# Kernel optimization log

Hardware: AMD Instinct MI355X
Metric: run time of the kernel (lower is better)

Reference implementation:

```python
import jax, jax.numpy as jnp
import numpy as np

B, S, E, NUM_CLASSES = 4, 4096, 256, 16

def setup_inputs() -> dict:
    key = jax.random.key(0)
    ks = jax.random.split(key, 10)
    std = E ** -0.5
    return {
        "x":  jax.random.normal(ks[0], (B, S, E), dtype=jnp.float32),
        "wq": jax.random.normal(ks[1], (E, E), dtype=jnp.float32) * std,
        "bq": jnp.zeros((E,), dtype=jnp.float32),
        "wk": jax.random.normal(ks[2], (E, E), dtype=jnp.float32) * std,
        "bk": jnp.zeros((E,), dtype=jnp.float32),
        "wv": jax.random.normal(ks[3], (E, E), dtype=jnp.float32) * std,
        "bv": jnp.zeros((E,), dtype=jnp.float32),
        "wo": jax.random.normal(ks[4], (NUM_CLASSES, E), dtype=jnp.float32) * std,
        "bo": jnp.zeros((NUM_CLASSES,), dtype=jnp.float32),
    }

def reference(x, wq, bq, wk, bk, wv, bv, wo, bo):
    embed_dim = wq.shape[0]
    scaling = embed_dim ** -0.5  # float(embed_dim) ** (-0.5)
    # torch Linear: y = x @ W.T + b
    Q = jnp.einsum('bse,oe->bso', x, wq) + bq
    K = jnp.einsum('bse,oe->bso', x, wk) + bk
    V = jnp.einsum('bse,oe->bso', x, wv) + bv
    # scores: [B, S, S]
    scores = jnp.einsum('bqe,bke->bqk', Q, K) * scaling
    # original code has `/ (embed_dim ^ 0.5)`; intended math is / sqrt(embed_dim)
    attn = jax.nn.softmax(scores, axis=-1) * scaling
    attn_out = jnp.einsum('bqk,bke->bqe', attn, V)
    return jnp.einsum('bqe,oe->bqo', attn_out, wo) + bo
```

## Files before the change

### kernel.cpp

```cpp
#include <hip/hip_runtime.h>
#include <hip/hip_bf16.h>


#define S_ 4096
#define E_ 256
#define B_ 4
#define NC_ 16
#define BS_ (B_ * S_)
#define NS_ 4

typedef __attribute__((ext_vector_type(8))) short bf16x8;
typedef __attribute__((ext_vector_type(4))) float f32x4;

__device__ __forceinline__ unsigned short bf16_rtne(float f) {
    unsigned int u = __float_as_uint(f);
    return (unsigned short)((u + 0x7FFFu + ((u >> 16) & 1u)) >> 16);
}
__device__ __forceinline__ bf16x8 pack8(f32x4 a, f32x4 b) {
    bf16x8 r;
#pragma unroll
    for (int i = 0; i < 4; i++) r[i] = (short)bf16_rtne(a[i]);
#pragma unroll
    for (int i = 0; i < 4; i++) r[4 + i] = (short)bf16_rtne(b[i]);
    return r;
}
__device__ __forceinline__ void gl_lds16(const void* g, void* lds) {
    __builtin_amdgcn_global_load_lds(
        (const __attribute__((address_space(1))) unsigned int*)g,
        (__attribute__((address_space(3))) unsigned int*)lds, 16, 0, 0);
}
__device__ __forceinline__ int swz_u(int q) { return q ^ ((q >> 3) & 7); }

#define WUNITS_ (3 * E_ * E_ / 8)
#define WOUNITS_ (NC_ * E_ / 8)
#define ZUNITS_ (BS_ * NC_ / 8)
__global__ __launch_bounds__(256) void pack_w(
    const float* __restrict__ wq, const float* __restrict__ wk,
    const float* __restrict__ wv, const float* __restrict__ wo,
    short* __restrict__ wb, short* __restrict__ wbo,
    float* __restrict__ partial) {
    int u = blockIdx.x * 256 + threadIdx.x;
    const float* src;
    short* dst;
    if (u < WUNITS_) {
        int sel = u >> 13;
        int off = (u & 8191) * 8;
        src = ((sel == 0) ? wq : (sel == 1) ? wk : wv) + off;
        dst = wb + sel * (E_ * E_) + off;
    } else if (u < WUNITS_ + WOUNITS_) {
        int u2 = u - WUNITS_;
        src = wo + (size_t)u2 * 8;
        dst = wbo + (size_t)u2 * 8;
    } else {
        int zu = u - (WUNITS_ + WOUNITS_);
        f32x4 z = {0.f, 0.f, 0.f, 0.f};
        ((f32x4*)partial)[zu * 2] = z;
        ((f32x4*)partial)[zu * 2 + 1] = z;
        return;
    }
    f32x4 a = *(const f32x4*)src;
    f32x4 b = *(const f32x4*)(src + 4);
    *(bf16x8*)dst = pack8(a, b);
}

__global__ __launch_bounds__(256) void qkv_gemm(
    const float* __restrict__ x, const short* __restrict__ wb,
    const float* __restrict__ bq, const float* __restrict__ bk,
    const float* __restrict__ bv, short* __restrict__ Qb,
    short* __restrict__ Kb, short* __restrict__ Vtc) {
    __shared__ __align__(16) short stg[2][8192];
    __shared__ __align__(16) short epi[16896];

    int t = threadIdx.x;
    int lin = blockIdx.x;
    int xcd = lin & 7, r8 = lin >> 3;
    int sel = r8 >> 5;
    int m0 = (((xcd << 5) | (r8 & 31))) * 64;
    int lane = t & 63, wid = t >> 6, quad = lane >> 4, idx = lane & 15;

    const short* wsel = wb + sel * (E_ * E_);
    const float* bias = (sel == 0) ? bq : (sel == 1) ? bk : bv;

    const short* wsrc[4];
#pragma unroll
    for (int i = 0; i < 4; i++) {
        int q = i * 256 + t, u = swz_u(q);
        wsrc[i] = wsel + (size_t)(u >> 2) * E_ + (u & 3) * 8;
    }

#pragma unroll
    for (int i = 0; i < 4; i++) gl_lds16(wsrc[i], &stg[0][(i * 256 + t) * 8]);

    const float* xrow = x + (size_t)(m0 + wid * 16 + idx) * E_ + quad * 8;
    bf16x8 af[8];
#pragma unroll
    for (int it = 0; it < 8; it++) {
        f32x4 a0 = *(const f32x4*)(xrow + it * 32);
        f32x4 a1 = *(const f32x4*)(xrow + it * 32 + 4);
        af[it] = pack8(a0, a1);
    }

    f32x4 zf = {0.f, 0.f, 0.f, 0.f};
    f32x4 acc[16];
#pragma unroll
    for (int i = 0; i < 16; i++) acc[i] = zf;

    int fo = (idx * 4 + quad) ^ (idx >> 1);

#pragma unroll
    for (int it = 0; it < 8; it++) {
        __syncthreads();
        if (it < 7) {
            int kc = (it + 1) * 32;
            short* d = stg[(it + 1) & 1];
#pragma unroll
            for (int i = 0; i < 4; i++)
                gl_lds16(wsrc[i] + kc, &d[(i * 256 + t) * 8]);
        }
        const short* cw = &stg[it & 1][fo * 8];
        __builtin_amdgcn_s_setprio(1);
#pragma unroll
        for (int ct = 0; ct < 16; ct++)
            acc[ct] = __builtin_amdgcn_mfma_f32_16x16x32_bf16(
                af[it], *(const bf16x8*)&cw[ct * 512], acc[ct], 0, 0, 0);
        __builtin_amdgcn_s_setprio(0);
    }

    int qr = quad * 4;
    if (sel == 2) {
#pragma unroll
        for (int ct = 0; ct < 16; ct++) {
            int e = ct * 16 + idx;
            float bb = bias[e];
#pragma unroll
            for (int r = 0; r < 4; r++) {
                int mr = wid * 16 + qr + r;
                int ckg = mr >> 5, sin = mr & 31;
                int sp = ((sin & 15) << 1) | (sin >> 4);
                int pos = (sp >> 3) ^ ((e >> 1) & 3);
                epi[ckg * 8192 + e * 32 + pos * 8 + (sp & 7)] =
                    (short)bf16_rtne(acc[ct][r] + bb);
            }
        }
        __syncthreads();
        size_t base = ((size_t)((m0 >> 12) * 128 + ((m0 & (S_ - 1)) >> 5))) * 8192;
#pragma unroll
        for (int j = 0; j < 8; j++) {
            int unit = j * 256 + t;
            *(bf16x8*)(Vtc + base + (size_t)unit * 8) = *(const bf16x8*)&epi[unit * 8];
        }
    } else {
        float alpha = (sel == 0) ? 0.0625f : 1.0f;
#pragma unroll
        for (int ct = 0; ct < 16; ct++) {
            int n = ct * 16 + idx;
            float bb = bias[n];
#pragma unroll
            for (int r = 0; r < 4; r++) {
                int row = wid * 16 + qr + r;
                int col = (sel == 1) ? ((((n >> 3) ^ (row & 7)) << 3) | (n & 7)) : n;
                epi[row * 264 + col] = (short)bf16_rtne((acc[ct][r] + bb) * alpha);
            }
        }
        __syncthreads();
        short* out = (sel == 0) ? Qb : Kb;
#pragma unroll
        for (int j = 0; j < 8; j++) {
            int g = j * 256 + t;
            int row = g >> 5, seg = g & 31;
            *(bf16x8*)(out + (size_t)(m0 + row) * E_ + seg * 8) =
                *(const bf16x8*)&epi[row * 264 + seg * 8];
        }
    }
}

__global__ __launch_bounds__(256, 2) void flash_attn(
    const short* __restrict__ Qb, const short* __restrict__ Kb,
    const short* __restrict__ Vtc, const short* __restrict__ wbo,
    float* __restrict__ partial, float* __restrict__ lpart) {
    __shared__ __align__(16) short lds[37888];

    int t = threadIdx.x;
    int lin = blockIdx.x;
    int xcd = lin & 7, r8 = lin >> 3;
    int pair = (xcd << 1) | (r8 >> 5);
    int b = pair >> 2, slice = pair & 3, q0 = (r8 & 31) * 128;
    int key0 = slice * (S_ / NS_);
    const int nchunk = (S_ / NS_) / 32;
    int lane = t & 63, wv = t >> 6, quad = lane >> 4, idx = lane & 15;

    bf16x8 qf[2][8];
#pragma unroll
    for (int u = 0; u < 2; u++) {
        const short* qrow = Qb + (size_t)(b * S_ + q0 + u * 64 + wv * 16 + idx) * E_ + quad * 8;
#pragma unroll
        for (int c = 0; c < 8; c++) qf[u][c] = *(const bf16x8*)(qrow + c * 32);
    }

    f32x4 zf = {0.f, 0.f, 0.f, 0.f};
    f32x4 oacc[2][16];
#pragma unroll
    for (int u = 0; u < 2; u++)
#pragma unroll
        for (int i = 0; i < 16; i++) oacc[u][i] = zf;
    float ls[2][4] = {{0, 0, 0, 0}, {0, 0, 0, 0}};

    const short* kg = Kb + (size_t)(b * S_ + key0) * E_ + lane * 8;
    const short* vg = Vtc + ((size_t)(b * 128 + (key0 >> 5))) * 8192 + lane * 8;
    short* psw = lds + 32768 + wv * 1280;
    unsigned int* pswu = (unsigned int*)psw;
    int vsw = (quad ^ ((idx >> 1) & 3)) << 3;

#pragma unroll
    for (int j = 0; j < 4; j++) gl_lds16(kg + (wv * 4 + j) * 512, &lds[(wv * 4 + j) * 512]);
#pragma unroll
    for (int j = 0; j < 4; j++) gl_lds16(vg + (wv * 4 + j) * 512, &lds[16384 + (wv * 4 + j) * 512]);
#pragma unroll
    for (int j = 0; j < 4; j++) gl_lds16(kg + 8192 + (wv * 4 + j) * 512, &lds[8192 + (wv * 4 + j) * 512]);
    __syncthreads();

    {
        f32x4 s[4] = {zf, zf, zf, zf};
        __builtin_amdgcn_s_setprio(1);
#pragma unroll
        for (int c = 0; c < 8; c++) {
            int p = (((c * 4 + quad) ^ (idx & 7)) << 3);
            bf16x8 k0 = *(const bf16x8*)&lds[idx * 256 + p];
            bf16x8 k1 = *(const bf16x8*)&lds[(16 + idx) * 256 + p];
            s[0] = __builtin_amdgcn_mfma_f32_16x16x32_bf16(qf[0][c], k0, s[0], 0, 0, 0);
            s[1] = __builtin_amdgcn_mfma_f32_16x16x32_bf16(qf[0][c], k1, s[1], 0, 0, 0);
            s[2] = __builtin_amdgcn_mfma_f32_16x16x32_bf16(qf[1][c], k0, s[2], 0, 0, 0);
            s[3] = __builtin_amdgcn_mfma_f32_16x16x32_bf16(qf[1][c], k1, s[3], 0, 0, 0);
        }
        __builtin_amdgcn_s_setprio(0);
#pragma unroll
        for (int u = 0; u < 2; u++)
#pragma unroll
            for (int r = 0; r < 4; r++) {
                float p0 = __expf(s[u * 2][r]);
                float p1 = __expf(s[u * 2 + 1][r]);
                ls[u][r] += p0 + p1;
                pswu[u * 320 + (quad * 4 + r) * 20 + idx] =
                    (unsigned int)bf16_rtne(p0) | ((unsigned int)bf16_rtne(p1) << 16);
            }
    }

    for (int ck = 0; ck < nchunk - 1; ck++) {
        __syncthreads();
        bf16x8 af0 = *(const bf16x8*)&psw[idx * 40 + quad * 8];
        bf16x8 af1 = *(const bf16x8*)&psw[640 + idx * 40 + quad * 8];
        if (ck + 2 < nchunk) {
            const short* ks = kg + (size_t)(ck + 2) * 8192;
            short* kd = lds + (ck & 1) * 8192;
#pragma unroll
            for (int j = 0; j < 4; j++) gl_lds16(ks + (wv * 4 + j) * 512, &kd[(wv * 4 + j) * 512]);
        }
        {
            const short* vs = vg + (size_t)(ck + 1) * 8192;
            short* vd = lds + 16384 + ((ck + 1) & 1) * 8192;
#pragma unroll
            for (int j = 0; j < 4; j++) gl_lds16(vs + (wv * 4 + j) * 512, &vd[(wv * 4 + j) * 512]);
        }
        const short* kc = lds + ((ck + 1) & 1) * 8192;
        f32x4 s[4] = {zf, zf, zf, zf};
        __builtin_amdgcn_s_setprio(1);
#pragma unroll
        for (int c = 0; c < 8; c++) {
            int p = (((c * 4 + quad) ^ (idx & 7)) << 3);
            bf16x8 k0 = *(const bf16x8*)&kc[idx * 256 + p];
            bf16x8 k1 = *(const bf16x8*)&kc[(16 + idx) * 256 + p];
            s[0] = __builtin_amdgcn_mfma_f32_16x16x32_bf16(qf[0][c], k0, s[0], 0, 0, 0);
            s[1] = __builtin_amdgcn_mfma_f32_16x16x32_bf16(qf[0][c], k1, s[1], 0, 0, 0);
            s[2] = __builtin_amdgcn_mfma_f32_16x16x32_bf16(qf[1][c], k0, s[2], 0, 0, 0);
            s[3] = __builtin_amdgcn_mfma_f32_16x16x32_bf16(qf[1][c], k1, s[3], 0, 0, 0);
        }
        __builtin_amdgcn_s_setprio(0);
#pragma unroll
        for (int u = 0; u < 2; u++)
#pragma unroll
            for (int r = 0; r < 4; r++) {
                float p0 = __expf(s[u * 2][r]);
                float p1 = __expf(s[u * 2 + 1][r]);
                ls[u][r] += p0 + p1;
                pswu[u * 320 + (quad * 4 + r) * 20 + idx] =
                    (unsigned int)bf16_rtne(p0) | ((unsigned int)bf16_rtne(p1) << 16);
            }
        const short* vc = lds + 16384 + (ck & 1) * 8192;
        __builtin_amdgcn_s_setprio(1);
#pragma unroll
        for (int ct = 0; ct < 16; ct++) {
            bf16x8 v = *(const bf16x8*)&vc[(ct * 16 + idx) * 32 + vsw];
            oacc[0][ct] = __builtin_amdgcn_mfma_f32_16x16x32_bf16(af0, v, oacc[0][ct], 0, 0, 0);
            oacc[1][ct] = __builtin_amdgcn_mfma_f32_16x16x32_bf16(af1, v, oacc[1][ct], 0, 0, 0);
        }
        __builtin_amdgcn_s_setprio(0);
    }
    __syncthreads();
    {
        bf16x8 af0 = *(const bf16x8*)&psw[idx * 40 + quad * 8];
        bf16x8 af1 = *(const bf16x8*)&psw[640 + idx * 40 + quad * 8];
        const short* vc = lds + 16384 + ((nchunk - 1) & 1) * 8192;
        __builtin_amdgcn_s_setprio(1);
#pragma unroll
        for (int ct = 0; ct < 16; ct++) {
            bf16x8 v = *(const bf16x8*)&vc[(ct * 16 + idx) * 32 + vsw];
            oacc[0][ct] = __builtin_amdgcn_mfma_f32_16x16x32_bf16(af0, v, oacc[0][ct], 0, 0, 0);
            oacc[1][ct] = __builtin_amdgcn_mfma_f32_16x16x32_bf16(af1, v, oacc[1][ct], 0, 0, 0);
        }
        __builtin_amdgcn_s_setprio(0);
    }
    __syncthreads();

#pragma unroll
    for (int u = 0; u < 2; u++)
#pragma unroll
        for (int r = 0; r < 4; r++) {
            float v = ls[u][r];
            v += __shfl_xor(v, 1);
            v += __shfl_xor(v, 2);
            v += __shfl_xor(v, 4);
            v += __shfl_xor(v, 8);
            if (idx == 0)
                lpart[(size_t)slice * BS_ + b * S_ + q0 + u * 64 + wv * 16 + quad * 4 + r] = v;
        }

    short* scr = lds + wv * 8192;
#pragma unroll
    for (int u = 0; u < 2; u++)
#pragma unroll
        for (int ct = 0; ct < 16; ct++) {
            int e = ct * 16 + idx;
#pragma unroll
            for (int r = 0; r < 4; r++) {
                int lr = quad * 4 + r;
                scr[u * 4096 + lr * 256 + ((((e >> 3) ^ (lr & 7)) << 3) | (e & 7))] =
                    (short)bf16_rtne(oacc[u][ct][r]);
            }
        }

    f32x4 pacc[2] = {zf, zf};
#pragma unroll
    for (int c = 0; c < 8; c++) {
        bf16x8 bw = *(const bf16x8*)(wbo + idx * E_ + c * 32 + quad * 8);
#pragma unroll
        for (int u = 0; u < 2; u++) {
            bf16x8 af = *(const bf16x8*)&scr[u * 4096 + idx * 256 +
                                             (((c * 4 + quad) ^ (idx & 7)) << 3)];
            pacc[u] = __builtin_amdgcn_mfma_f32_16x16x32_bf16(af, bw, pacc[u], 0, 0, 0);
        }
    }
#pragma unroll
    for (int u = 0; u < 2; u++)
#pragma unroll
        for (int r = 0; r < 4; r++) {
            int m = q0 + u * 64 + wv * 16 + quad * 4 + r;
            atomicAdd(&partial[((size_t)b * S_ + m) * NC_ + idx], pacc[u][r]);
        }
}

__global__ __launch_bounds__(256) void norm_out(
    const float* __restrict__ partial, const float* __restrict__ lpart,
    const float* __restrict__ bo, float* __restrict__ out) {
    int t = threadIdx.x;
    int m = blockIdx.x * 16 + (t >> 4), o = t & 15;
    float ltot = 0.f;
#pragma unroll
    for (int ns = 0; ns < NS_; ns++) ltot += lpart[(size_t)ns * BS_ + m];
    size_t i = (size_t)m * NC_ + o;
    out[i] = partial[i] * (0.0625f / ltot) + bo[o];
}

extern "C" void kernel_launch(void* const* d_in, const int* in_sizes, int n_in,
                              void* d_out, int out_size, void* d_ws, size_t ws_size,
                              hipStream_t stream) {
    const float* x  = (const float*)d_in[0];
    const float* wq = (const float*)d_in[1];
    const float* bq = (const float*)d_in[2];
    const float* wk = (const float*)d_in[3];
    const float* bk = (const float*)d_in[4];
    const float* wv = (const float*)d_in[5];
    const float* bv = (const float*)d_in[6];
    const float* wo = (const float*)d_in[7];
    const float* bo = (const float*)d_in[8];
    float* out = (float*)d_out;

    const size_t NEL = (size_t)BS_ * E_;
    short* Qb = (short*)d_ws;
    short* Kb = Qb + NEL;
    short* Vtc = Kb + NEL;
    short* wb = Vtc + NEL;
    short* wbo = wb + (size_t)3 * E_ * E_;
    float* partial = (float*)(wbo + (size_t)NC_ * E_);
    float* lpart = partial + (size_t)BS_ * NC_;

    pack_w<<<(WUNITS_ + WOUNITS_ + ZUNITS_) / 256, 256, 0, stream>>>(
        wq, wk, wv, wo, wb, wbo, partial);
    qkv_gemm<<<dim3(768), 256, 0, stream>>>(x, wb, bq, bk, bv, Qb, Kb, Vtc);
    flash_attn<<<dim3(512), 256, 0, stream>>>(Qb, Kb, Vtc, wbo, partial, lpart);
    norm_out<<<dim3(BS_ / 16), 256, 0, stream>>>(partial, lpart, bo, out);
}
```

Measured before the change: 169.9 us.

## Double query tile per flash-attention block to 256 rows for more K/V reuse

Each flash_attn block now handles 256 query rows (4 sub-tiles per wave) instead of 128, which halves the grid to 256 blocks and sets launch bounds to 1 block per SM. Every K/V chunk staged into LDS is now reused across twice as many MFMAs, cutting global and LDS traffic per unit of work. In exchange, register pressure roughly doubles (Q fragments and accumulators), occupancy drops, and the smaller grid may leave compute units underfilled. The output projection epilogue is split into two passes to fit the scratch space.

```diff
diff --git a/kernel.cpp b/kernel.cpp
--- a/kernel.cpp
+++ b/kernel.cpp
@@ -174,40 +174,40 @@
     }
 }
 
-__global__ __launch_bounds__(256, 2) void flash_attn(
+__global__ __launch_bounds__(256, 1) void flash_attn(
     const short* __restrict__ Qb, const short* __restrict__ Kb,
     const short* __restrict__ Vtc, const short* __restrict__ wbo,
     float* __restrict__ partial, float* __restrict__ lpart) {
-    __shared__ __align__(16) short lds[37888];
+    __shared__ __align__(16) short lds[43008];
 
     int t = threadIdx.x;
     int lin = blockIdx.x;
-    int xcd = lin & 7, r8 = lin >> 3;
-    int pair = (xcd << 1) | (r8 >> 5);
-    int b = pair >> 2, slice = pair & 3, q0 = (r8 & 31) * 128;
+    int xcd = lin & 7, r5 = lin >> 3;
+    int pair = (xcd << 1) | (r5 >> 4);
+    int b = pair >> 2, slice = pair & 3, q0 = (r5 & 15) * 256;
     int key0 = slice * (S_ / NS_);
     const int nchunk = (S_ / NS_) / 32;
     int lane = t & 63, wv = t >> 6, quad = lane >> 4, idx = lane & 15;
 
-    bf16x8 qf[2][8];
-#pragma unroll
-    for (int u = 0; u < 2; u++) {
+    bf16x8 qf[4][8];
+#pragma unroll
+    for (int u = 0; u < 4; u++) {
         const short* qrow = Qb + (size_t)(b * S_ + q0 + u * 64 + wv * 16 + idx) * E_ + quad * 8;
 #pragma unroll
         for (int c = 0; c < 8; c++) qf[u][c] = *(const bf16x8*)(qrow + c * 32);
     }
 
     f32x4 zf = {0.f, 0.f, 0.f, 0.f};
-    f32x4 oacc[2][16];
-#pragma unroll
-    for (int u = 0; u < 2; u++)
+    f32x4 oacc[4][16];
+#pragma unroll
+    for (int u = 0; u < 4; u++)
 #pragma unroll
         for (int i = 0; i < 16; i++) oacc[u][i] = zf;
-    float ls[2][4] = {{0, 0, 0, 0}, {0, 0, 0, 0}};
+    float ls[4][4] = {{0, 0, 0, 0}, {0, 0, 0, 0}, {0, 0, 0, 0}, {0, 0, 0, 0}};
 
     const short* kg = Kb + (size_t)(b * S_ + key0) * E_ + lane * 8;
     const short* vg = Vtc + ((size_t)(b * 128 + (key0 >> 5))) * 8192 + lane * 8;
-    short* psw = lds + 32768 + wv * 1280;
+    short* psw = lds + 32768 + wv * 2560;
     unsigned int* pswu = (unsigned int*)psw;
     int vsw = (quad ^ ((idx >> 1) & 3)) << 3;
 
@@ -220,21 +220,22 @@
     __syncthreads();
 
     {
-        f32x4 s[4] = {zf, zf, zf, zf};
+        f32x4 s[8] = {zf, zf, zf, zf, zf, zf, zf, zf};
         __builtin_amdgcn_s_setprio(1);
 #pragma unroll
         for (int c = 0; c < 8; c++) {
             int p = (((c * 4 + quad) ^ (idx & 7)) << 3);
             bf16x8 k0 = *(const bf16x8*)&lds[idx * 256 + p];
             bf16x8 k1 = *(const bf16x8*)&lds[(16 + idx) * 256 + p];
-            s[0] = __builtin_amdgcn_mfma_f32_16x16x32_bf16(qf[0][c], k0, s[0], 0, 0, 0);
-            s[1] = __builtin_amdgcn_mfma_f32_16x16x32_bf16(qf[0][c], k1, s[1], 0, 0, 0);
-            s[2] = __builtin_amdgcn_mfma_f32_16x16x32_bf16(qf[1][c], k0, s[2], 0, 0, 0);
-            s[3] = __builtin_amdgcn_mfma_f32_16x16x32_bf16(qf[1][c], k1, s[3], 0, 0, 0);
+#pragma unroll
+            for (int u = 0; u < 4; u++) {
+                s[u * 2] = __builtin_amdgcn_mfma_f32_16x16x32_bf16(qf[u][c], k0, s[u * 2], 0, 0, 0);
+                s[u * 2 + 1] = __builtin_amdgcn_mfma_f32_16x16x32_bf16(qf[u][c], k1, s[u * 2 + 1], 0, 0, 0);
+            }
         }
         __builtin_amdgcn_s_setprio(0);
 #pragma unroll
-        for (int u = 0; u < 2; u++)
+        for (int u = 0; u < 4; u++)
 #pragma unroll
             for (int r = 0; r < 4; r++) {
                 float p0 = __expf(s[u * 2][r]);
@@ -247,8 +248,10 @@
 
     for (int ck = 0; ck < nchunk - 1; ck++) {
         __syncthreads();
-        bf16x8 af0 = *(const bf16x8*)&psw[idx * 40 + quad * 8];
-        bf16x8 af1 = *(const bf16x8*)&psw[640 + idx * 40 + quad * 8];
+        bf16x8 af[4];
+#pragma unroll
+        for (int u = 0; u < 4; u++)
+            af[u] = *(const bf16x8*)&psw[u * 640 + idx * 40 + quad * 8];
         if (ck + 2 < nchunk) {
             const short* ks = kg + (size_t)(ck + 2) * 8192;
             short* kd = lds + (ck & 1) * 8192;
@@ -262,21 +265,22 @@
             for (int j = 0; j < 4; j++) gl_lds16(vs + (wv * 4 + j) * 512, &vd[(wv * 4 + j) * 512]);
         }
         const short* kc = lds + ((ck + 1) & 1) * 8192;
-        f32x4 s[4] = {zf, zf, zf, zf};
+        f32x4 s[8] = {zf, zf, zf, zf, zf, zf, zf, zf};
         __builtin_amdgcn_s_setprio(1);
 #pragma unroll
         for (int c = 0; c < 8; c++) {
             int p = (((c * 4 + quad) ^ (idx & 7)) << 3);
             bf16x8 k0 = *(const bf16x8*)&kc[idx * 256 + p];
             bf16x8 k1 = *(const bf16x8*)&kc[(16 + idx) * 256 + p];
-            s[0] = __builtin_amdgcn_mfma_f32_16x16x32_bf16(qf[0][c], k0, s[0], 0, 0, 0);
-            s[1] = __builtin_amdgcn_mfma_f32_16x16x32_bf16(qf[0][c], k1, s[1], 0, 0, 0);
-            s[2] = __builtin_amdgcn_mfma_f32_16x16x32_bf16(qf[1][c], k0, s[2], 0, 0, 0);
-            s[3] = __builtin_amdgcn_mfma_f32_16x16x32_bf16(qf[1][c], k1, s[3], 0, 0, 0);
+#pragma unroll
+            for (int u = 0; u < 4; u++) {
+                s[u * 2] = __builtin_amdgcn_mfma_f32_16x16x32_bf16(qf[u][c], k0, s[u * 2], 0, 0, 0);
+                s[u * 2 + 1] = __builtin_amdgcn_mfma_f32_16x16x32_bf16(qf[u][c], k1, s[u * 2 + 1], 0, 0, 0);
+            }
         }
         __builtin_amdgcn_s_setprio(0);
 #pragma unroll
-        for (int u = 0; u < 2; u++)
+        for (int u = 0; u < 4; u++)
 #pragma unroll
             for (int r = 0; r < 4; r++) {
                 float p0 = __expf(s[u * 2][r]);
@@ -290,29 +294,33 @@
 #pragma unroll
         for (int ct = 0; ct < 16; ct++) {
             bf16x8 v = *(const bf16x8*)&vc[(ct * 16 + idx) * 32 + vsw];
-            oacc[0][ct] = __builtin_amdgcn_mfma_f32_16x16x32_bf16(af0, v, oacc[0][ct], 0, 0, 0);
-            oacc[1][ct] = __builtin_amdgcn_mfma_f32_16x16x32_bf16(af1, v, oacc[1][ct], 0, 0, 0);
+#pragma unroll
+            for (int u = 0; u < 4; u++)
+                oacc[u][ct] = __builtin_amdgcn_mfma_f32_16x16x32_bf16(af[u], v, oacc[u][ct], 0, 0, 0);
         }
         __builtin_amdgcn_s_setprio(0);
     }
     __syncthreads();
     {
-        bf16x8 af0 = *(const bf16x8*)&psw[idx * 40 + quad * 8];
-        bf16x8 af1 = *(const bf16x8*)&psw[640 + idx * 40 + quad * 8];
+        bf16x8 af[4];
+#pragma unroll
+        for (int u = 0; u < 4; u++)
+            af[u] = *(const bf16x8*)&psw[u * 640 + idx * 40 + quad * 8];
         const short* vc = lds + 16384 + ((nchunk - 1) & 1) * 8192;
         __builtin_amdgcn_s_setprio(1);
 #pragma unroll
         for (int ct = 0; ct < 16; ct++) {
             bf16x8 v = *(const bf16x8*)&vc[(ct * 16 + idx) * 32 + vsw];
-            oacc[0][ct] = __builtin_amdgcn_mfma_f32_16x16x32_bf16(af0, v, oacc[0][ct], 0, 0, 0);
-            oacc[1][ct] = __builtin_amdgcn_mfma_f32_16x16x32_bf16(af1, v, oacc[1][ct], 0, 0, 0);
+#pragma unroll
+            for (int u = 0; u < 4; u++)
+                oacc[u][ct] = __builtin_amdgcn_mfma_f32_16x16x32_bf16(af[u], v, oacc[u][ct], 0, 0, 0);
         }
         __builtin_amdgcn_s_setprio(0);
     }
     __syncthreads();
 
 #pragma unroll
-    for (int u = 0; u < 2; u++)
+    for (int u = 0; u < 4; u++)
 #pragma unroll
         for (int r = 0; r < 4; r++) {
             float v = ls[u][r];
@@ -326,36 +334,40 @@
 
     short* scr = lds + wv * 8192;
 #pragma unroll
-    for (int u = 0; u < 2; u++)
-#pragma unroll
-        for (int ct = 0; ct < 16; ct++) {
-            int e = ct * 16 + idx;
+    for (int up = 0; up < 2; up++) {
+#pragma unroll
+        for (int uu = 0; uu < 2; uu++) {
+            int u = up * 2 + uu;
+#pragma unroll
+            for (int ct = 0; ct < 16; ct++) {
+                int e = ct * 16 + idx;
+#pragma unroll
+                for (int r = 0; r < 4; r++) {
+                    int lr = quad * 4 + r;
+                    scr[uu * 4096 + lr * 256 + ((((e >> 3) ^ (lr & 7)) << 3) | (e & 7))] =
+                        (short)bf16_rtne(oacc[u][ct][r]);
+                }
+            }
+        }
+        f32x4 pacc[2] = {zf, zf};
+#pragma unroll
+        for (int c = 0; c < 8; c++) {
+            bf16x8 bw = *(const bf16x8*)(wbo + idx * E_ + c * 32 + quad * 8);
+#pragma unroll
+            for (int uu = 0; uu < 2; uu++) {
+                bf16x8 pa = *(const bf16x8*)&scr[uu * 4096 + idx * 256 +
+                                                 (((c * 4 + quad) ^ (idx & 7)) << 3)];
+                pacc[uu] = __builtin_amdgcn_mfma_f32_16x16x32_bf16(pa, bw, pacc[uu], 0, 0, 0);
+            }
+        }
+#pragma unroll
+        for (int uu = 0; uu < 2; uu++)
 #pragma unroll
             for (int r = 0; r < 4; r++) {
-                int lr = quad * 4 + r;
-                scr[u * 4096 + lr * 256 + ((((e >> 3) ^ (lr & 7)) << 3) | (e & 7))] =
-                    (short)bf16_rtne(oacc[u][ct][r]);
-            }
-        }
-
-    f32x4 pacc[2] = {zf, zf};
-#pragma unroll
-    for (int c = 0; c < 8; c++) {
-        bf16x8 bw = *(const bf16x8*)(wbo + idx * E_ + c * 32 + quad * 8);
-#pragma unroll
-        for (int u = 0; u < 2; u++) {
-            bf16x8 af = *(const bf16x8*)&scr[u * 4096 + idx * 256 +
-                                             (((c * 4 + quad) ^ (idx & 7)) << 3)];
-            pacc[u] = __builtin_amdgcn_mfma_f32_16x16x32_bf16(af, bw, pacc[u], 0, 0, 0);
-        }
-    }
-#pragma unroll
-    for (int u = 0; u < 2; u++)
-#pragma unroll
-        for (int r = 0; r < 4; r++) {
-            int m = q0 + u * 64 + wv * 16 + quad * 4 + r;
-            atomicAdd(&partial[((size_t)b * S_ + m) * NC_ + idx], pacc[u][r]);
-        }
+                int m = q0 + (up * 2 + uu) * 64 + wv * 16 + quad * 4 + r;
+                atomicAdd(&partial[((size_t)b * S_ + m) * NC_ + idx], pacc[uu][r]);
+            }
+    }
 }
 
 __global__ __launch_bounds__(256) void norm_out(
@@ -396,6 +408,6 @@
     pack_w<<<(WUNITS_ + WOUNITS_ + ZUNITS_) / 256, 256, 0, stream>>>(
         wq, wk, wv, wo, wb, wbo, partial);
     qkv_gemm<<<dim3(768), 256, 0, stream>>>(x, wb, bq, bk, bv, Qb, Kb, Vtc);
-    flash_attn<<<dim3(512), 256, 0, stream>>>(Qb, Kb, Vtc, wbo, partial, lpart);
+    flash_attn<<<dim3(256), 256, 0, stream>>>(Qb, Kb, Vtc, wbo, partial, lpart);
     norm_out<<<dim3(BS_ / 16), 256, 0, stream>>>(partial, lpart, bo, out);
 }
```

After: 192.0 us. +13.0%, slower.

## Fuse weight packing and partial zeroing into the QKV GEMM and attention

Applied to the files above, without the earlier changes.

Removes the separate pack_w kernel. The QKV GEMM now loads fp32 weights into registers, converts them to bf16 and stores them into the LDS double buffer, replacing the async global-to-LDS bf16 copies. It also zeroes the partial-output buffer. The attention epilogue converts wo from fp32 on the fly. This saves one kernel launch and a round trip through the workspace, at the cost of each GEMM block re-converting weights and moving weight staging from the async LDS path to register loads, which may weaken load/compute overlap.

```diff
diff --git a/kernel.cpp b/kernel.cpp
--- a/kernel.cpp
+++ b/kernel.cpp
@@ -31,43 +31,13 @@
 }
 __device__ __forceinline__ int swz_u(int q) { return q ^ ((q >> 3) & 7); }
 
-#define WUNITS_ (3 * E_ * E_ / 8)
-#define WOUNITS_ (NC_ * E_ / 8)
-#define ZUNITS_ (BS_ * NC_ / 8)
-__global__ __launch_bounds__(256) void pack_w(
-    const float* __restrict__ wq, const float* __restrict__ wk,
-    const float* __restrict__ wv, const float* __restrict__ wo,
-    short* __restrict__ wb, short* __restrict__ wbo,
-    float* __restrict__ partial) {
-    int u = blockIdx.x * 256 + threadIdx.x;
-    const float* src;
-    short* dst;
-    if (u < WUNITS_) {
-        int sel = u >> 13;
-        int off = (u & 8191) * 8;
-        src = ((sel == 0) ? wq : (sel == 1) ? wk : wv) + off;
-        dst = wb + sel * (E_ * E_) + off;
-    } else if (u < WUNITS_ + WOUNITS_) {
-        int u2 = u - WUNITS_;
-        src = wo + (size_t)u2 * 8;
-        dst = wbo + (size_t)u2 * 8;
-    } else {
-        int zu = u - (WUNITS_ + WOUNITS_);
-        f32x4 z = {0.f, 0.f, 0.f, 0.f};
-        ((f32x4*)partial)[zu * 2] = z;
-        ((f32x4*)partial)[zu * 2 + 1] = z;
-        return;
-    }
-    f32x4 a = *(const f32x4*)src;
-    f32x4 b = *(const f32x4*)(src + 4);
-    *(bf16x8*)dst = pack8(a, b);
-}
-
 __global__ __launch_bounds__(256) void qkv_gemm(
-    const float* __restrict__ x, const short* __restrict__ wb,
+    const float* __restrict__ x, const float* __restrict__ wq,
+    const float* __restrict__ wk, const float* __restrict__ wv,
     const float* __restrict__ bq, const float* __restrict__ bk,
     const float* __restrict__ bv, short* __restrict__ Qb,
-    short* __restrict__ Kb, short* __restrict__ Vtc) {
+    short* __restrict__ Kb, short* __restrict__ Vtc,
+    float* __restrict__ partial) {
     __shared__ __align__(16) short stg[2][8192];
     __shared__ __align__(16) short epi[16896];
 
@@ -78,18 +48,28 @@
     int m0 = (((xcd << 5) | (r8 & 31))) * 64;
     int lane = t & 63, wid = t >> 6, quad = lane >> 4, idx = lane & 15;
 
-    const short* wsel = wb + sel * (E_ * E_);
+    const float* wsel = (sel == 0) ? wq : (sel == 1) ? wk : wv;
     const float* bias = (sel == 0) ? bq : (sel == 1) ? bk : bv;
 
-    const short* wsrc[4];
+    const float* wsrc[4];
 #pragma unroll
     for (int i = 0; i < 4; i++) {
         int q = i * 256 + t, u = swz_u(q);
         wsrc[i] = wsel + (size_t)(u >> 2) * E_ + (u & 3) * 8;
     }
 
-#pragma unroll
-    for (int i = 0; i < 4; i++) gl_lds16(wsrc[i], &stg[0][(i * 256 + t) * 8]);
+    f32x4 wf[8];
+#pragma unroll
+    for (int i = 0; i < 4; i++) {
+        wf[i * 2] = *(const f32x4*)(wsrc[i]);
+        wf[i * 2 + 1] = *(const f32x4*)(wsrc[i] + 4);
+    }
+
+    {
+        int z = lin * 256 + t;
+        partial[z] = 0.f;
+        if (z < BS_ * NC_ - 196608) partial[z + 196608] = 0.f;
+    }
 
     const float* xrow = x + (size_t)(m0 + wid * 16 + idx) * E_ + quad * 8;
     bf16x8 af[8];
@@ -100,6 +80,10 @@
         af[it] = pack8(a0, a1);
     }
 
+#pragma unroll
+    for (int i = 0; i < 4; i++)
+        *(bf16x8*)&stg[0][(i * 256 + t) * 8] = pack8(wf[i * 2], wf[i * 2 + 1]);
+
     f32x4 zf = {0.f, 0.f, 0.f, 0.f};
     f32x4 acc[16];
 #pragma unroll
@@ -107,15 +91,17 @@
 
     int fo = (idx * 4 + quad) ^ (idx >> 1);
 
+    __syncthreads();
+
 #pragma unroll
     for (int it = 0; it < 8; it++) {
-        __syncthreads();
         if (it < 7) {
             int kc = (it + 1) * 32;
-            short* d = stg[(it + 1) & 1];
-#pragma unroll
-            for (int i = 0; i < 4; i++)
-                gl_lds16(wsrc[i] + kc, &d[(i * 256 + t) * 8]);
+#pragma unroll
+            for (int i = 0; i < 4; i++) {
+                wf[i * 2] = *(const f32x4*)(wsrc[i] + kc);
+                wf[i * 2 + 1] = *(const f32x4*)(wsrc[i] + kc + 4);
+            }
         }
         const short* cw = &stg[it & 1][fo * 8];
         __builtin_amdgcn_s_setprio(1);
@@ -124,6 +110,13 @@
             acc[ct] = __builtin_amdgcn_mfma_f32_16x16x32_bf16(
                 af[it], *(const bf16x8*)&cw[ct * 512], acc[ct], 0, 0, 0);
         __builtin_amdgcn_s_setprio(0);
+        if (it < 7) {
+            short* d = stg[(it + 1) & 1];
+#pragma unroll
+            for (int i = 0; i < 4; i++)
+                *(bf16x8*)&d[(i * 256 + t) * 8] = pack8(wf[i * 2], wf[i * 2 + 1]);
+        }
+        __syncthreads();
     }
 
     int qr = quad * 4;
@@ -176,7 +169,7 @@
 
 __global__ __launch_bounds__(256, 2) void flash_attn(
     const short* __restrict__ Qb, const short* __restrict__ Kb,
-    const short* __restrict__ Vtc, const short* __restrict__ wbo,
+    const short* __restrict__ Vtc, const float* __restrict__ wo,
     float* __restrict__ partial, float* __restrict__ lpart) {
     __shared__ __align__(16) short lds[37888];
 
@@ -341,12 +334,13 @@
     f32x4 pacc[2] = {zf, zf};
 #pragma unroll
     for (int c = 0; c < 8; c++) {
-        bf16x8 bw = *(const bf16x8*)(wbo + idx * E_ + c * 32 + quad * 8);
+        const float* ws = wo + idx * E_ + c * 32 + quad * 8;
+        bf16x8 bw = pack8(*(const f32x4*)ws, *(const f32x4*)(ws + 4));
 #pragma unroll
         for (int u = 0; u < 2; u++) {
-            bf16x8 af = *(const bf16x8*)&scr[u * 4096 + idx * 256 +
+            bf16x8 pa = *(const bf16x8*)&scr[u * 4096 + idx * 256 +
                                              (((c * 4 + quad) ^ (idx & 7)) << 3)];
-            pacc[u] = __builtin_amdgcn_mfma_f32_16x16x32_bf16(af, bw, pacc[u], 0, 0, 0);
+            pacc[u] = __builtin_amdgcn_mfma_f32_16x16x32_bf16(pa, bw, pacc[u], 0, 0, 0);
         }
     }
 #pragma unroll
@@ -388,14 +382,10 @@
     short* Qb = (short*)d_ws;
     short* Kb = Qb + NEL;
     short* Vtc = Kb + NEL;
-    short* wb = Vtc + NEL;
-    short* wbo = wb + (size_t)3 * E_ * E_;
-    float* partial = (float*)(wbo + (size_t)NC_ * E_);
+    float* partial = (float*)(Vtc + NEL);
     float* lpart = partial + (size_t)BS_ * NC_;
 
-    pack_w<<<(WUNITS_ + WOUNITS_ + ZUNITS_) / 256, 256, 0, stream>>>(
-        wq, wk, wv, wo, wb, wbo, partial);
-    qkv_gemm<<<dim3(768), 256, 0, stream>>>(x, wb, bq, bk, bv, Qb, Kb, Vtc);
-    flash_attn<<<dim3(512), 256, 0, stream>>>(Qb, Kb, Vtc, wbo, partial, lpart);
+    qkv_gemm<<<dim3(768), 256, 0, stream>>>(x, wq, wk, wv, bq, bk, bv, Qb, Kb, Vtc, partial);
+    flash_attn<<<dim3(512), 256, 0, stream>>>(Qb, Kb, Vtc, wo, partial, lpart);
     norm_out<<<dim3(BS_ / 16), 256, 0, stream>>>(partial, lpart, bo, out);
 }
```

After: 172.6 us. About the same (+1.6%).
